# Kernel optimization log

Hardware: AMD Instinct MI355X
Metric: run time of the kernel (lower is better)

## Reference

```python
import jax, jax.numpy as jnp
import numpy as np

R = 4           # max_displacement
P = 2 * R + 1   # search_range = 9
DILATIONS = [[1], [1, 2, 3, 5, 9, 16]]
STRIDES = [4, 1]  # 8 // encoder_output_stride for strides [2, 8]
EPS = 1e-9


def _l2norm(x):
    # torch: x / (x.norm(dim=1, keepdim=True) + 1e-9)
    return x / (jnp.linalg.norm(x, axis=1, keepdims=True) + EPS)


def _corr(x1, x2, dilation, stride):
    """SpatialCorrelationSampler(patch_size=9, stride=stride, padding=0,
    dilation_patch=dilation): out[b,u,v,i,j] = sum_c x1[b,c,i*s,j*s] *
    x2[b,c,i*s+(u-R)*d, j*s+(v-R)*d], zero outside bounds."""
    B, C, H, W = x1.shape
    pad = R * dilation
    x2p = jnp.pad(x2, ((0, 0), (0, 0), (pad, pad), (pad, pad)))
    x1s = x1[:, :, ::stride, ::stride]  # (B,C,Ho,Wo)
    Ho, Wo = x1s.shape[2], x1s.shape[3]
    # all 81 (u,v) patch-offset slice starts in the padded map
    uv = jnp.stack(jnp.meshgrid(jnp.arange(P), jnp.arange(P), indexing='ij'),
                   axis=-1).reshape(-1, 2) * dilation  # (81, 2)

    def step(carry, start):
        x2uv = jax.lax.dynamic_slice(x2p, (0, 0, start[0], start[1]), (B, C, H, W))
        x2uv = x2uv[:, :, ::stride, ::stride]
        return carry, jnp.sum(x1s * x2uv, axis=1)  # (B,Ho,Wo)

    _, cost = jax.lax.scan(step, None, uv)  # (81,B,Ho,Wo)
    cost = cost.reshape(P, P, B, Ho, Wo)
    return jnp.transpose(cost, (2, 0, 1, 3, 4))  # (B,P,P,Ho,Wo)


def setup_inputs() -> dict:
    key = jax.random.key(0)
    k0, k1, k2, k3 = jax.random.split(key, 4)
    return {
        'x1_0': jax.random.normal(k0, (4, 256, 192, 256), dtype=jnp.float32),
        'x1_1': jax.random.normal(k1, (4, 256, 48, 64), dtype=jnp.float32),
        'x2_0': jax.random.normal(k2, (4, 256, 192, 256), dtype=jnp.float32),
        'x2_1': jax.random.normal(k3, (4, 256, 48, 64), dtype=jnp.float32),
    }


def reference(x1_0, x1_1, x2_0, x2_1):
    xs1, xs2 = [x1_0, x1_1], [x2_0, x2_1]
    cost_list = []
    for x1, x2, dils, s in zip(xs1, xs2, DILATIONS, STRIDES):
        x1n = _l2norm(x1)
        x2n = _l2norm(x2)
        per_dil = [_corr(x1n, x2n, d, s) for d in dils]  # each (B,P,P,Ho,Wo)
        # num_groups=1: per-dilation volumes stack into dim 1
        cost_list.append(jnp.stack(per_dil, axis=1))  # (B,nd,P,P,Ho,Wo)
    return jnp.concatenate(cost_list, axis=1)  # (B,7,9,9,48,64)
```

## Files before the change

kernel.cpp:

```cpp
#include <hip/hip_runtime.h>
#include <stdint.h>

#define EPSN 1e-9f

typedef __fp16 f16x8 __attribute__((ext_vector_type(8)));
typedef float f32x4 __attribute__((ext_vector_type(4)));

#define LDS_FENCE()                                        \
  do {                                                     \
    asm volatile("s_waitcnt lgkmcnt(0)" ::: "memory");     \
    __builtin_amdgcn_sched_barrier(0);                     \
  } while (0)


__global__ __launch_bounds__(256) void norms1_kernel(
    const float* __restrict__ x1_1, const float* __restrict__ x2_1,
    float* __restrict__ ws) {
  int p = blockIdx.x * 256 + threadIdx.x;
  const float* src = (p < 12288) ? x1_1 : x2_1;
  int q = (p < 12288) ? p : p - 12288;
  long base = (long)(q / 3072) * 786432 + (q % 3072);
  float ss = 0.f;
#pragma unroll 8
  for (int c = 0; c < 256; ++c) { float v = src[base + (long)c * 3072]; ss += v * v; }
  ws[p] = 1.f / (sqrtf(ss) + EPSN);
}

__global__ __launch_bounds__(256) void gather1_kernel(
    const float* __restrict__ x1, float* __restrict__ x1s) {
  int idx = blockIdx.x * 256 + threadIdx.x;
  int j = idx & 63;
  int i = (idx >> 6) % 48;
  int c = ((idx >> 6) / 48) & 255;
  int b = idx >> 19;
  b = idx / 786432;
  x1s[idx] = x1[(long)b * 12582912 + (long)c * 49152 + (long)(4 * i) * 256 + 4 * j];
}

__global__ __launch_bounds__(256) void corr0_kernel(
    const float* __restrict__ x1b, long BS, long RS, int CS, long CCS,
    const float* __restrict__ x2, float* __restrict__ out) {
  int bx = blockIdx.x;
  int L = (bx & 7) * 96 + (bx >> 3);
  int y = L % 192, b = L / 192;
  int tid = threadIdx.x;
  int w = tid >> 6, lane = tid & 63;
  int i_lo = (y - 1) / 4; if (i_lo < 0) i_lo = 0;
  int i_hi = (y + 4) / 4; if (i_hi > 47) i_hi = 47;
  int NI = i_hi - i_lo + 1;

  __shared__ float red[4][34][64];
  __shared__ float inv2s[264];
  __shared__ float inv1s[3][64];

  float acc[3][9];
#pragma unroll
  for (int r = 0; r < 3; ++r)
#pragma unroll
    for (int v = 0; v < 9; ++v) acc[r][v] = 0.f;
  float sq0 = 0.f, sq1 = 0.f, sq2 = 0.f, sq3 = 0.f;
  float s1[3] = {0.f, 0.f, 0.f};

  const float* x2row = x2 + (long)b * 12582912 + (long)y * 256 + 4 * lane;
  const float* x1p[3];
#pragma unroll
  for (int r = 0; r < 3; ++r) {
    int ir = i_lo + r; if (ir > 47) ir = 47;
    x1p[r] = x1b + (long)b * BS + (long)ir * RS + (long)lane * CS;
  }

#pragma unroll 4
  for (int cc = 0; cc < 64; ++cc) {
    int c = w * 64 + cc;
    long off2 = (long)c * 49152;
    long off1 = (long)c * CCS;
    float4 f = *reinterpret_cast<const float4*>(x2row + off2);
    sq0 += f.x * f.x; sq1 += f.y * f.y; sq2 += f.z * f.z; sq3 += f.w * f.w;
#pragma unroll
    for (int r = 0; r < 3; ++r) {
      float xv = x1p[r][off1];
      float xr = __shfl_down(xv, 1);
      float xl = __shfl_up(xv, 1);
      s1[r] += xv * xv;
      acc[r][0] += xr * f.x; acc[r][1] += xr * f.y;
      acc[r][2] += xr * f.z; acc[r][3] += xr * f.w;
      acc[r][4] += xv * f.x; acc[r][5] += xv * f.y;
      acc[r][6] += xv * f.z; acc[r][7] += xv * f.w;
      acc[r][8] += xl * f.x;
    }
  }

#pragma unroll
  for (int r = 0; r < 3; ++r) {
    red[w][r * 9 + 0][lane] = __shfl_up(acc[r][0], 1);
    red[w][r * 9 + 1][lane] = __shfl_up(acc[r][1], 1);
    red[w][r * 9 + 2][lane] = __shfl_up(acc[r][2], 1);
    red[w][r * 9 + 3][lane] = __shfl_up(acc[r][3], 1);
    red[w][r * 9 + 4][lane] = acc[r][4];
    red[w][r * 9 + 5][lane] = acc[r][5];
    red[w][r * 9 + 6][lane] = acc[r][6];
    red[w][r * 9 + 7][lane] = acc[r][7];
    red[w][r * 9 + 8][lane] = __shfl_down(acc[r][8], 1);
    red[w][31 + r][lane] = s1[r];
  }
  red[w][27][lane] = sq0; red[w][28][lane] = sq1;
  red[w][29][lane] = sq2; red[w][30][lane] = sq3;
  __syncthreads();
  {
    int comp = tid & 3, jj = tid >> 2;
    float ss = red[0][27 + comp][jj] + red[1][27 + comp][jj] +
               red[2][27 + comp][jj] + red[3][27 + comp][jj];
    inv2s[4 + tid] = 1.f / (sqrtf(ss) + EPSN);
    if (tid < 4) { inv2s[tid] = 0.f; inv2s[260 + tid] = 0.f; }
    if (tid < 192) {
      int r = tid >> 6, j = tid & 63;
      float t = red[0][31 + r][j] + red[1][31 + r][j] +
                red[2][31 + r][j] + red[3][31 + r][j];
      inv1s[r][j] = 1.f / (sqrtf(t) + EPSN);
    }
  }
  __syncthreads();
  int lim = NI * 576;
  for (int idx = tid; idx < lim; idx += 256) {
    int r = idx / 576, rem = idx - r * 576;
    int v = rem >> 6, j = rem & 63;
    int i_r = i_lo + r;
    int u_r = y - 4 * i_r + 4;
    float s = red[0][r * 9 + v][j] + red[1][r * 9 + v][j] +
              red[2][r * 9 + v][j] + red[3][r * 9 + v][j];
    out[(long)b * 1741824 + (long)u_r * 27648 + (long)v * 3072 + i_r * 64 + j] =
        s * inv1s[r][j] * inv2s[4 * j + v];
  }
}

__global__ __launch_bounds__(256) void zfill0_kernel(float* __restrict__ out) {
  int idx = blockIdx.x * 256 + threadIdx.x;
  int b = idx / 2880, rem = idx - b * 2880;
  int k = rem / 576, rem2 = rem - k * 576;
  int v = rem2 >> 6, j = rem2 & 63;
  int u = (k < 4) ? k : 8;
  int i = (k < 4) ? 0 : 47;
  out[(long)b * 1741824 + (long)u * 27648 + (long)v * 3072 + i * 64 + j] = 0.f;
}

__global__ __launch_bounds__(256) void xpose1_kernel(
    const float* __restrict__ x1, const float* __restrict__ x2,
    __fp16* __restrict__ o1, __fp16* __restrict__ o2) {
  int bx = blockIdx.x;
  int tz = bx & 1; int rem = bx >> 1;
  int i = rem % 48, b = rem / 48;
  const float* src = tz ? x2 : x1;
  __fp16* dst = (tz ? o2 : o1) + (long)(b * 48 + i) * 16384;
  __shared__ uint32_t lds[64 * 128];
  __shared__ float sred[4][64];
  int t = threadIdx.x;
  int j = t & 63, cg = t >> 6;
  const float* sp = src + (long)b * 786432 + (long)i * 64 + j;
  float vv[64];
  float ss = 0.f;
#pragma unroll
  for (int c8 = 0; c8 < 64; ++c8) {
    float v = sp[(long)(cg * 64 + c8) * 3072];
    vv[c8] = v;
    ss += v * v;
  }
  sred[cg][j] = ss;
  __syncthreads();
  float invv = 1.f / (sqrtf(sred[0][j] + sred[1][j] + sred[2][j] + sred[3][j]) + EPSN);
#pragma unroll
  for (int cb = 0; cb < 8; ++cb) {
    uint32_t pk[4];
#pragma unroll
    for (int e2 = 0; e2 < 4; ++e2) {
      int cl = cb * 8 + e2 * 2;
      __fp16 h0 = (__fp16)(vv[cl] * invv);
      __fp16 h1 = (__fp16)(vv[cl + 1] * invv);
      pk[e2] = (uint32_t)__builtin_bit_cast(uint16_t, h0) |
               ((uint32_t)__builtin_bit_cast(uint16_t, h1) << 16);
    }
    int byteoff = j * 512 + ((cg * 128 + cb * 16) ^ ((j & 7) << 4));
    *reinterpret_cast<uint4*>(reinterpret_cast<char*>(lds) + byteoff) =
        make_uint4(pk[0], pk[1], pk[2], pk[3]);
  }
  __syncthreads();
#pragma unroll
  for (int rep = 0; rep < 8; ++rep) {
    int idx = rep * 256 + t;
    int jj = idx >> 5, cb = idx & 31;
    int byteoff = jj * 512 + ((cb * 16) ^ ((jj & 7) << 4));
    uint4 val = *reinterpret_cast<const uint4*>(
        reinterpret_cast<const char*>(lds) + byteoff);
    *reinterpret_cast<uint4*>(reinterpret_cast<char*>(dst) + jj * 512 + cb * 16) = val;
  }
}

__device__ const int OFFS39[39] = {
    0, 1, -1, 2, -2, 3, -3, 4, -4, 5, -5, 6, -6, 8, -8, 9, -9, 10, -10,
    12, -12, 15, -15, 16, -16, 18, -18, 20, -20, 27, -27, 32, -32, 36, -36,
    48, -48, 64, -64};

__global__ __launch_bounds__(64) void corr1m_kernel(
    const __fp16* __restrict__ w1, const __fp16* __restrict__ w2,
    float* __restrict__ out) {
  const int dils[6] = {1, 2, 3, 5, 9, 16};
  int bx = blockIdx.x;
  int L = (bx & 7) * 936 + (bx >> 3);
  int oi = L % 39, i = (L / 39) % 48, b = L / 1872;
  int o = OFFS39[oi];
  int y = i + o;
  bool valid = (y >= 0 && y < 48);
  int l = threadIdx.x;
  __shared__ float c_lds[64][65];

  if (valid) {
    int lm = l & 15, lk = l >> 4;
    const __fp16* A = w1 + (long)(b * 48 + i) * 16384;
    const __fp16* B = w2 + (long)(b * 48 + y) * 16384;
    f32x4 acc[4][4];
#pragma unroll
    for (int tm = 0; tm < 4; ++tm)
#pragma unroll
      for (int tn = 0; tn < 4; ++tn) acc[tm][tn] = (f32x4)0.f;

    for (int ks = 0; ks < 8; ++ks) {
      f16x8 af[4], bf[4];
      int ko = ks * 32 + lk * 8;
#pragma unroll
      for (int tm = 0; tm < 4; ++tm)
        af[tm] = __builtin_bit_cast(f16x8, *reinterpret_cast<const uint4*>(
                     A + (tm * 16 + lm) * 256 + ko));
#pragma unroll
      for (int tn = 0; tn < 4; ++tn)
        bf[tn] = __builtin_bit_cast(f16x8, *reinterpret_cast<const uint4*>(
                     B + (tn * 16 + lm) * 256 + ko));
#pragma unroll
      for (int tm = 0; tm < 4; ++tm)
#pragma unroll
        for (int tn = 0; tn < 4; ++tn)
          acc[tm][tn] = __builtin_amdgcn_mfma_f32_16x16x32_f16(
              af[tm], bf[tn], acc[tm][tn], 0, 0, 0);
    }
#pragma unroll
    for (int tm = 0; tm < 4; ++tm)
#pragma unroll
      for (int tn = 0; tn < 4; ++tn)
#pragma unroll
        for (int r = 0; r < 4; ++r)
          c_lds[tm * 16 + lk * 4 + r][tn * 16 + lm] = acc[tm][tn][r];
    LDS_FENCE();
  }

#pragma unroll
  for (int dI = 0; dI < 6; ++dI) {
    int d = dils[dI];
    if (o % d) continue;
    int ud = o / d;
    if (ud < -4 || ud > 4) continue;
    long ob = (long)b * 1741824 + (long)(1 + dI) * 248832 +
              (long)(ud + 4) * 27648 + (long)i * 64 + l;
#pragma unroll
    for (int v = 0; v < 9; ++v) {
      float val = 0.f;
      if (valid) {
        int j2 = l + (v - 4) * d;
        val = (j2 >= 0 && j2 < 64) ? c_lds[l][j2] : 0.f;
      }
      out[ob + (long)v * 3072] = val;
    }
  }
}

__global__ __launch_bounds__(64) void corr1_kernel(
    const float* __restrict__ x1, const float* __restrict__ x2,
    const float* __restrict__ ws, float* __restrict__ out) {
  int bx = blockIdx.x;
  int L = (bx & 7) * 1296 + (bx >> 3);
  int u = L % 9, dI = (L / 9) % 6, i = (L / 54) % 48, b = L / 2592;
  const int dils[6] = {1, 2, 3, 5, 9, 16};
  int d = dils[dI];
  int y = i + (u - 4) * d;
  int lane = threadIdx.x;
  long ob = (long)b * 1741824 + (long)(1 + dI) * 248832 + (long)u * 27648 +
            (long)i * 64 + lane;
  if (y < 0 || y >= 48) {
#pragma unroll
    for (int v = 0; v < 9; ++v) out[ob + v * 3072] = 0.f;
    return;
  }
  __shared__ uint4 x2t[192];
  x2t[lane] = make_uint4(0, 0, 0, 0);
  x2t[lane + 64] = make_uint4(0, 0, 0, 0);
  x2t[lane + 128] = make_uint4(0, 0, 0, 0);
  float acc[9];
#pragma unroll
  for (int v = 0; v < 9; ++v) acc[v] = 0.f;
  const float* x2row = x2 + (long)b * 786432 + (long)y * 64 + lane;
  const float* x1row = x1 + (long)b * 786432 + (long)i * 64 + lane;
#pragma unroll 1
  for (int cc8 = 0; cc8 < 32; ++cc8) {
    float x1v[8]; uint32_t xb[8];
#pragma unroll
    for (int cc = 0; cc < 8; ++cc) {
      long c = cc8 * 8 + cc;
      xb[cc] = __float_as_uint(x2row[c * 3072]) + 0x8000u;
      x1v[cc] = x1row[c * 3072];
    }
    uint4 pk;
    pk.x = (xb[0] >> 16) | (xb[1] & 0xffff0000u);
    pk.y = (xb[2] >> 16) | (xb[3] & 0xffff0000u);
    pk.z = (xb[4] >> 16) | (xb[5] & 0xffff0000u);
    pk.w = (xb[6] >> 16) | (xb[7] & 0xffff0000u);
    x2t[64 + lane] = pk;
    LDS_FENCE();
#pragma unroll
    for (int v = 0; v < 9; ++v) {
      uint4 q = x2t[64 + lane + (v - 4) * d];
      float s;
      s  = x1v[0] * __uint_as_float(q.x << 16);
      s += x1v[1] * __uint_as_float(q.x & 0xffff0000u);
      s += x1v[2] * __uint_as_float(q.y << 16);
      s += x1v[3] * __uint_as_float(q.y & 0xffff0000u);
      s += x1v[4] * __uint_as_float(q.z << 16);
      s += x1v[5] * __uint_as_float(q.z & 0xffff0000u);
      s += x1v[6] * __uint_as_float(q.w << 16);
      s += x1v[7] * __uint_as_float(q.w & 0xffff0000u);
      acc[v] += s;
    }
    LDS_FENCE();
  }
  const float* i1 = ws + b * 3072 + i * 64;
  const float* i2 = ws + 12288 + b * 3072 + y * 64;
  float inv1 = i1[lane];
#pragma unroll
  for (int v = 0; v < 9; ++v) {
    int col = lane + (v - 4) * d;
    float i2v = (col >= 0 && col < 64) ? i2[col] : 0.f;
    out[ob + v * 3072] = acc[v] * inv1 * i2v;
  }
}

extern "C" void kernel_launch(void* const* d_in, const int* in_sizes, int n_in,
                              void* d_out, int out_size, void* d_ws, size_t ws_size,
                              hipStream_t stream) {
  const float* x1_0 = (const float*)d_in[0];
  const float* x1_1 = (const float*)d_in[1];
  const float* x2_0 = (const float*)d_in[2];
  const float* x2_1 = (const float*)d_in[3];
  float* out = (float*)d_out;
  float* ws = (float*)d_ws;
  if (ws_size >= 25264128) {
    float* x1s = (float*)((char*)d_ws + 12681216);
    gather1_kernel<<<12288, 256, 0, stream>>>(x1_0, x1s);
    corr0_kernel<<<768, 256, 0, stream>>>(x1s, 786432L, 64L, 1, 3072L,
                                          x2_0, out);
  } else {
    corr0_kernel<<<768, 256, 0, stream>>>(x1_0, 12582912L, 1024L, 4, 49152L,
                                          x2_0, out);
  }
  zfill0_kernel<<<45, 256, 0, stream>>>(out);
  if (ws_size >= 12681216) {
    __fp16* w1h = (__fp16*)((char*)d_ws + 98304);
    __fp16* w2h = w1h + 3145728;
    xpose1_kernel<<<384, 256, 0, stream>>>(x1_1, x2_1, w1h, w2h);
    corr1m_kernel<<<7488, 64, 0, stream>>>(w1h, w2h, out);
  } else {
    norms1_kernel<<<96, 256, 0, stream>>>(x1_1, x2_1, ws);
    corr1_kernel<<<10368, 64, 0, stream>>>(x1_1, x2_1, ws, out);
  }
}
```

Baseline: 118.5 us.

## Split corr0 channel loop across eight waves with two-phase LDS reduction

corr0_kernel now launches 512 threads (8 waves), and each wave handles 32 channels instead of 64. This halves the serial channel loop per thread and adds more waves per block to hide the latency of streaming the large x2_0 tensor. The cross-wave reduction buffer shrinks to 8x14x64 floats and is reused in two passes (14 and 13 accumulator rows), which adds extra barriers and reduction reads. Launch bounds are set to (512,4), which may constrain registers.

```diff
diff --git a/kernel.cpp b/kernel.cpp
--- a/kernel.cpp
+++ b/kernel.cpp
@@ -32,12 +32,11 @@
   int j = idx & 63;
   int i = (idx >> 6) % 48;
   int c = ((idx >> 6) / 48) & 255;
-  int b = idx >> 19;
-  b = idx / 786432;
+  int b = idx / 786432;
   x1s[idx] = x1[(long)b * 12582912 + (long)c * 49152 + (long)(4 * i) * 256 + 4 * j];
 }
 
-__global__ __launch_bounds__(256) void corr0_kernel(
+__global__ __launch_bounds__(512, 4) void corr0_kernel(
     const float* __restrict__ x1b, long BS, long RS, int CS, long CCS,
     const float* __restrict__ x2, float* __restrict__ out) {
   int bx = blockIdx.x;
@@ -49,7 +48,7 @@
   int i_hi = (y + 4) / 4; if (i_hi > 47) i_hi = 47;
   int NI = i_hi - i_lo + 1;
 
-  __shared__ float red[4][34][64];
+  __shared__ float red[8][14][64];
   __shared__ float inv2s[264];
   __shared__ float inv1s[3][64];
 
@@ -70,8 +69,8 @@
   }
 
 #pragma unroll 4
-  for (int cc = 0; cc < 64; ++cc) {
-    int c = w * 64 + cc;
+  for (int cc = 0; cc < 32; ++cc) {
+    int c = w * 32 + cc;
     long off2 = (long)c * 49152;
     long off1 = (long)c * CCS;
     float4 f = *reinterpret_cast<const float4*>(x2row + off2);
@@ -92,44 +91,72 @@
 
 #pragma unroll
   for (int r = 0; r < 3; ++r) {
-    red[w][r * 9 + 0][lane] = __shfl_up(acc[r][0], 1);
-    red[w][r * 9 + 1][lane] = __shfl_up(acc[r][1], 1);
-    red[w][r * 9 + 2][lane] = __shfl_up(acc[r][2], 1);
-    red[w][r * 9 + 3][lane] = __shfl_up(acc[r][3], 1);
-    red[w][r * 9 + 4][lane] = acc[r][4];
-    red[w][r * 9 + 5][lane] = acc[r][5];
-    red[w][r * 9 + 6][lane] = acc[r][6];
-    red[w][r * 9 + 7][lane] = acc[r][7];
-    red[w][r * 9 + 8][lane] = __shfl_down(acc[r][8], 1);
-    red[w][31 + r][lane] = s1[r];
-  }
-  red[w][27][lane] = sq0; red[w][28][lane] = sq1;
-  red[w][29][lane] = sq2; red[w][30][lane] = sq3;
-  __syncthreads();
-  {
+    acc[r][0] = __shfl_up(acc[r][0], 1);
+    acc[r][1] = __shfl_up(acc[r][1], 1);
+    acc[r][2] = __shfl_up(acc[r][2], 1);
+    acc[r][3] = __shfl_up(acc[r][3], 1);
+    acc[r][8] = __shfl_down(acc[r][8], 1);
+  }
+
+  red[w][0][lane] = sq0; red[w][1][lane] = sq1;
+  red[w][2][lane] = sq2; red[w][3][lane] = sq3;
+  red[w][4][lane] = s1[0]; red[w][5][lane] = s1[1]; red[w][6][lane] = s1[2];
+  __syncthreads();
+  if (tid < 256) {
     int comp = tid & 3, jj = tid >> 2;
-    float ss = red[0][27 + comp][jj] + red[1][27 + comp][jj] +
-               red[2][27 + comp][jj] + red[3][27 + comp][jj];
+    float ss = 0.f;
+#pragma unroll
+    for (int ww = 0; ww < 8; ++ww) ss += red[ww][comp][jj];
     inv2s[4 + tid] = 1.f / (sqrtf(ss) + EPSN);
-    if (tid < 4) { inv2s[tid] = 0.f; inv2s[260 + tid] = 0.f; }
-    if (tid < 192) {
-      int r = tid >> 6, j = tid & 63;
-      float t = red[0][31 + r][j] + red[1][31 + r][j] +
-                red[2][31 + r][j] + red[3][31 + r][j];
-      inv1s[r][j] = 1.f / (sqrtf(t) + EPSN);
-    }
-  }
-  __syncthreads();
-  int lim = NI * 576;
-  for (int idx = tid; idx < lim; idx += 256) {
-    int r = idx / 576, rem = idx - r * 576;
-    int v = rem >> 6, j = rem & 63;
-    int i_r = i_lo + r;
-    int u_r = y - 4 * i_r + 4;
-    float s = red[0][r * 9 + v][j] + red[1][r * 9 + v][j] +
-              red[2][r * 9 + v][j] + red[3][r * 9 + v][j];
-    out[(long)b * 1741824 + (long)u_r * 27648 + (long)v * 3072 + i_r * 64 + j] =
-        s * inv1s[r][j] * inv2s[4 * j + v];
+  } else if (tid < 264) {
+    int e = tid - 256;
+    inv2s[(e < 4) ? e : (256 + e)] = 0.f;
+  } else if (tid >= 320) {
+    int r = (tid - 320) >> 6, j = tid & 63;
+    float t = 0.f;
+#pragma unroll
+    for (int ww = 0; ww < 8; ++ww) t += red[ww][4 + r][j];
+    inv1s[r][j] = 1.f / (sqrtf(t) + EPSN);
+  }
+  __syncthreads();
+
+#pragma unroll
+  for (int ar = 0; ar < 14; ++ar) {
+    int r = (ar >= 9) ? 1 : 0, v = ar - r * 9;
+    red[w][ar][lane] = acc[r][v];
+  }
+  __syncthreads();
+  for (int idx = tid; idx < 14 * 64; idx += 512) {
+    int ar = idx >> 6, j = idx & 63;
+    int r = (ar >= 9) ? 1 : 0, v = ar - r * 9;
+    if (r < NI) {
+      float s = 0.f;
+#pragma unroll
+      for (int ww = 0; ww < 8; ++ww) s += red[ww][ar][j];
+      int i_r = i_lo + r, u_r = y - 4 * i_r + 4;
+      out[(long)b * 1741824 + (long)u_r * 27648 + (long)v * 3072 + i_r * 64 + j] =
+          s * inv1s[r][j] * inv2s[4 * j + v];
+    }
+  }
+  __syncthreads();
+
+#pragma unroll
+  for (int ar = 14; ar < 27; ++ar) {
+    int r = (ar >= 18) ? 2 : 1, v = ar - r * 9;
+    red[w][ar - 14][lane] = acc[r][v];
+  }
+  __syncthreads();
+  for (int idx = tid; idx < 13 * 64; idx += 512) {
+    int ar = 14 + (idx >> 6), j = idx & 63;
+    int r = (ar >= 18) ? 2 : 1, v = ar - r * 9;
+    if (r < NI) {
+      float s = 0.f;
+#pragma unroll
+      for (int ww = 0; ww < 8; ++ww) s += red[ww][ar - 14][j];
+      int i_r = i_lo + r, u_r = y - 4 * i_r + 4;
+      out[(long)b * 1741824 + (long)u_r * 27648 + (long)v * 3072 + i_r * 64 + j] =
+          s * inv1s[r][j] * inv2s[4 * j + v];
+    }
   }
 }
 
@@ -351,10 +378,10 @@
   if (ws_size >= 25264128) {
     float* x1s = (float*)((char*)d_ws + 12681216);
     gather1_kernel<<<12288, 256, 0, stream>>>(x1_0, x1s);
-    corr0_kernel<<<768, 256, 0, stream>>>(x1s, 786432L, 64L, 1, 3072L,
+    corr0_kernel<<<768, 512, 0, stream>>>(x1s, 786432L, 64L, 1, 3072L,
                                           x2_0, out);
   } else {
-    corr0_kernel<<<768, 256, 0, stream>>>(x1_0, 12582912L, 1024L, 4, 49152L,
+    corr0_kernel<<<768, 512, 0, stream>>>(x1_0, 12582912L, 1024L, 4, 49152L,
                                           x2_0, out);
   }
   zfill0_kernel<<<45, 256, 0, stream>>>(out);
```

Measured after the change: 129.2 us. 9.0% more time.

## Fuse stride-2 correlation, dilated MFMA correlation and zero-fill into one launch

Applied to the files above, without the earlier changes.

Merges the level-0 correlation kernel, the level-1 multi-dilation MFMA correlation and the border zero-fill into a single kernel that dispatches on block index. The aim is to remove launch gaps and let the small level-1 blocks fill the GPU alongside the 768 level-0 blocks. The MFMA part is also reshaped from one 64-thread wave computing a 64x64 tile to four waves each computing a 16-row strip, which synchronises through a block barrier. In exchange, every block now reserves the larger LDS footprint and the 256-thread launch bound, and three of the four waves sit idle during the output write of the level-1 path.

```diff
diff --git a/kernel.cpp b/kernel.cpp
--- a/kernel.cpp
+++ b/kernel.cpp
@@ -32,115 +32,8 @@
   int j = idx & 63;
   int i = (idx >> 6) % 48;
   int c = ((idx >> 6) / 48) & 255;
-  int b = idx >> 19;
-  b = idx / 786432;
+  int b = idx / 786432;
   x1s[idx] = x1[(long)b * 12582912 + (long)c * 49152 + (long)(4 * i) * 256 + 4 * j];
-}
-
-__global__ __launch_bounds__(256) void corr0_kernel(
-    const float* __restrict__ x1b, long BS, long RS, int CS, long CCS,
-    const float* __restrict__ x2, float* __restrict__ out) {
-  int bx = blockIdx.x;
-  int L = (bx & 7) * 96 + (bx >> 3);
-  int y = L % 192, b = L / 192;
-  int tid = threadIdx.x;
-  int w = tid >> 6, lane = tid & 63;
-  int i_lo = (y - 1) / 4; if (i_lo < 0) i_lo = 0;
-  int i_hi = (y + 4) / 4; if (i_hi > 47) i_hi = 47;
-  int NI = i_hi - i_lo + 1;
-
-  __shared__ float red[4][34][64];
-  __shared__ float inv2s[264];
-  __shared__ float inv1s[3][64];
-
-  float acc[3][9];
-#pragma unroll
-  for (int r = 0; r < 3; ++r)
-#pragma unroll
-    for (int v = 0; v < 9; ++v) acc[r][v] = 0.f;
-  float sq0 = 0.f, sq1 = 0.f, sq2 = 0.f, sq3 = 0.f;
-  float s1[3] = {0.f, 0.f, 0.f};
-
-  const float* x2row = x2 + (long)b * 12582912 + (long)y * 256 + 4 * lane;
-  const float* x1p[3];
-#pragma unroll
-  for (int r = 0; r < 3; ++r) {
-    int ir = i_lo + r; if (ir > 47) ir = 47;
-    x1p[r] = x1b + (long)b * BS + (long)ir * RS + (long)lane * CS;
-  }
-
-#pragma unroll 4
-  for (int cc = 0; cc < 64; ++cc) {
-    int c = w * 64 + cc;
-    long off2 = (long)c * 49152;
-    long off1 = (long)c * CCS;
-    float4 f = *reinterpret_cast<const float4*>(x2row + off2);
-    sq0 += f.x * f.x; sq1 += f.y * f.y; sq2 += f.z * f.z; sq3 += f.w * f.w;
-#pragma unroll
-    for (int r = 0; r < 3; ++r) {
-      float xv = x1p[r][off1];
-      float xr = __shfl_down(xv, 1);
-      float xl = __shfl_up(xv, 1);
-      s1[r] += xv * xv;
-      acc[r][0] += xr * f.x; acc[r][1] += xr * f.y;
-      acc[r][2] += xr * f.z; acc[r][3] += xr * f.w;
-      acc[r][4] += xv * f.x; acc[r][5] += xv * f.y;
-      acc[r][6] += xv * f.z; acc[r][7] += xv * f.w;
-      acc[r][8] += xl * f.x;
-    }
-  }
-
-#pragma unroll
-  for (int r = 0; r < 3; ++r) {
-    red[w][r * 9 + 0][lane] = __shfl_up(acc[r][0], 1);
-    red[w][r * 9 + 1][lane] = __shfl_up(acc[r][1], 1);
-    red[w][r * 9 + 2][lane] = __shfl_up(acc[r][2], 1);
-    red[w][r * 9 + 3][lane] = __shfl_up(acc[r][3], 1);
-    red[w][r * 9 + 4][lane] = acc[r][4];
-    red[w][r * 9 + 5][lane] = acc[r][5];
-    red[w][r * 9 + 6][lane] = acc[r][6];
-    red[w][r * 9 + 7][lane] = acc[r][7];
-    red[w][r * 9 + 8][lane] = __shfl_down(acc[r][8], 1);
-    red[w][31 + r][lane] = s1[r];
-  }
-  red[w][27][lane] = sq0; red[w][28][lane] = sq1;
-  red[w][29][lane] = sq2; red[w][30][lane] = sq3;
-  __syncthreads();
-  {
-    int comp = tid & 3, jj = tid >> 2;
-    float ss = red[0][27 + comp][jj] + red[1][27 + comp][jj] +
-               red[2][27 + comp][jj] + red[3][27 + comp][jj];
-    inv2s[4 + tid] = 1.f / (sqrtf(ss) + EPSN);
-    if (tid < 4) { inv2s[tid] = 0.f; inv2s[260 + tid] = 0.f; }
-    if (tid < 192) {
-      int r = tid >> 6, j = tid & 63;
-      float t = red[0][31 + r][j] + red[1][31 + r][j] +
-                red[2][31 + r][j] + red[3][31 + r][j];
-      inv1s[r][j] = 1.f / (sqrtf(t) + EPSN);
-    }
-  }
-  __syncthreads();
-  int lim = NI * 576;
-  for (int idx = tid; idx < lim; idx += 256) {
-    int r = idx / 576, rem = idx - r * 576;
-    int v = rem >> 6, j = rem & 63;
-    int i_r = i_lo + r;
-    int u_r = y - 4 * i_r + 4;
-    float s = red[0][r * 9 + v][j] + red[1][r * 9 + v][j] +
-              red[2][r * 9 + v][j] + red[3][r * 9 + v][j];
-    out[(long)b * 1741824 + (long)u_r * 27648 + (long)v * 3072 + i_r * 64 + j] =
-        s * inv1s[r][j] * inv2s[4 * j + v];
-  }
-}
-
-__global__ __launch_bounds__(256) void zfill0_kernel(float* __restrict__ out) {
-  int idx = blockIdx.x * 256 + threadIdx.x;
-  int b = idx / 2880, rem = idx - b * 2880;
-  int k = rem / 576, rem2 = rem - k * 576;
-  int v = rem2 >> 6, j = rem2 & 63;
-  int u = (k < 4) ? k : 8;
-  int i = (k < 4) ? 0 : 47;
-  out[(long)b * 1741824 + (long)u * 27648 + (long)v * 3072 + i * 64 + j] = 0.f;
 }
 
 __global__ __launch_bounds__(256) void xpose1_kernel(
@@ -199,6 +92,270 @@
     12, -12, 15, -15, 16, -16, 18, -18, 20, -20, 27, -27, 32, -32, 36, -36,
     48, -48, 64, -64};
 
+__global__ __launch_bounds__(256) void corr_fused_kernel(
+    const float* __restrict__ x1s, const float* __restrict__ x2,
+    const __fp16* __restrict__ w1h, const __fp16* __restrict__ w2h,
+    float* __restrict__ out) {
+  __shared__ float smem[9160];
+  int bxg = blockIdx.x;
+  int tid = threadIdx.x;
+
+  if (bxg < 768) {
+    int L = (bxg & 7) * 96 + (bxg >> 3);
+    int y = L % 192, b = L / 192;
+    int w = tid >> 6, lane = tid & 63;
+    int i_lo = (y - 1) / 4; if (i_lo < 0) i_lo = 0;
+    int i_hi = (y + 4) / 4; if (i_hi > 47) i_hi = 47;
+    int NI = i_hi - i_lo + 1;
+    float (*red)[34][64] = reinterpret_cast<float(*)[34][64]>(smem);
+    float* inv2s = smem + 8704;
+    float (*inv1s)[64] = reinterpret_cast<float(*)[64]>(smem + 8968);
+
+    float acc[3][9];
+#pragma unroll
+    for (int r = 0; r < 3; ++r)
+#pragma unroll
+      for (int v = 0; v < 9; ++v) acc[r][v] = 0.f;
+    float sq0 = 0.f, sq1 = 0.f, sq2 = 0.f, sq3 = 0.f;
+    float s1[3] = {0.f, 0.f, 0.f};
+
+    const float* x2row = x2 + (long)b * 12582912 + (long)y * 256 + 4 * lane;
+    const float* x1p[3];
+#pragma unroll
+    for (int r = 0; r < 3; ++r) {
+      int ir = i_lo + r; if (ir > 47) ir = 47;
+      x1p[r] = x1s + (long)b * 786432 + (long)ir * 64 + lane;
+    }
+
+#pragma unroll 4
+    for (int cc = 0; cc < 64; ++cc) {
+      int c = w * 64 + cc;
+      float4 f = *reinterpret_cast<const float4*>(x2row + (long)c * 49152);
+      long off1 = (long)c * 3072;
+      sq0 += f.x * f.x; sq1 += f.y * f.y; sq2 += f.z * f.z; sq3 += f.w * f.w;
+#pragma unroll
+      for (int r = 0; r < 3; ++r) {
+        float xv = x1p[r][off1];
+        float xr = __shfl_down(xv, 1);
+        float xl = __shfl_up(xv, 1);
+        s1[r] += xv * xv;
+        acc[r][0] += xr * f.x; acc[r][1] += xr * f.y;
+        acc[r][2] += xr * f.z; acc[r][3] += xr * f.w;
+        acc[r][4] += xv * f.x; acc[r][5] += xv * f.y;
+        acc[r][6] += xv * f.z; acc[r][7] += xv * f.w;
+        acc[r][8] += xl * f.x;
+      }
+    }
+
+#pragma unroll
+    for (int r = 0; r < 3; ++r) {
+      red[w][r * 9 + 0][lane] = __shfl_up(acc[r][0], 1);
+      red[w][r * 9 + 1][lane] = __shfl_up(acc[r][1], 1);
+      red[w][r * 9 + 2][lane] = __shfl_up(acc[r][2], 1);
+      red[w][r * 9 + 3][lane] = __shfl_up(acc[r][3], 1);
+      red[w][r * 9 + 4][lane] = acc[r][4];
+      red[w][r * 9 + 5][lane] = acc[r][5];
+      red[w][r * 9 + 6][lane] = acc[r][6];
+      red[w][r * 9 + 7][lane] = acc[r][7];
+      red[w][r * 9 + 8][lane] = __shfl_down(acc[r][8], 1);
+      red[w][31 + r][lane] = s1[r];
+    }
+    red[w][27][lane] = sq0; red[w][28][lane] = sq1;
+    red[w][29][lane] = sq2; red[w][30][lane] = sq3;
+    __syncthreads();
+    {
+      int comp = tid & 3, jj = tid >> 2;
+      float ss = red[0][27 + comp][jj] + red[1][27 + comp][jj] +
+                 red[2][27 + comp][jj] + red[3][27 + comp][jj];
+      inv2s[4 + tid] = 1.f / (sqrtf(ss) + EPSN);
+      if (tid < 4) { inv2s[tid] = 0.f; inv2s[260 + tid] = 0.f; }
+      if (tid < 192) {
+        int r = tid >> 6, j = tid & 63;
+        float t = red[0][31 + r][j] + red[1][31 + r][j] +
+                  red[2][31 + r][j] + red[3][31 + r][j];
+        inv1s[r][j] = 1.f / (sqrtf(t) + EPSN);
+      }
+    }
+    __syncthreads();
+    int lim = NI * 576;
+    for (int idx = tid; idx < lim; idx += 256) {
+      int r = idx / 576, rem = idx - r * 576;
+      int v = rem >> 6, j = rem & 63;
+      int i_r = i_lo + r;
+      int u_r = y - 4 * i_r + 4;
+      float s = red[0][r * 9 + v][j] + red[1][r * 9 + v][j] +
+                red[2][r * 9 + v][j] + red[3][r * 9 + v][j];
+      out[(long)b * 1741824 + (long)u_r * 27648 + (long)v * 3072 + i_r * 64 + j] =
+          s * inv1s[r][j] * inv2s[4 * j + v];
+    }
+  } else if (bxg < 8256) {
+    const int dils[6] = {1, 2, 3, 5, 9, 16};
+    int s = bxg - 768;
+    int L = (s & 7) * 936 + (s >> 3);
+    int oi = L % 39, i = (L / 39) % 48, b = L / 1872;
+    int o = OFFS39[oi];
+    int y = i + o;
+    bool valid = (y >= 0 && y < 48);
+    int l = tid & 63, w = tid >> 6;
+    float (*c_lds)[65] = reinterpret_cast<float(*)[65]>(smem);
+
+    if (valid) {
+      int lm = l & 15, lk = l >> 4;
+      const __fp16* A = w1h + (long)(b * 48 + i) * 16384;
+      const __fp16* B = w2h + (long)(b * 48 + y) * 16384;
+      f32x4 acc[4];
+#pragma unroll
+      for (int tn = 0; tn < 4; ++tn) acc[tn] = (f32x4)0.f;
+      for (int ks = 0; ks < 8; ++ks) {
+        int ko = ks * 32 + lk * 8;
+        f16x8 af = __builtin_bit_cast(f16x8, *reinterpret_cast<const uint4*>(
+                       A + (w * 16 + lm) * 256 + ko));
+#pragma unroll
+        for (int tn = 0; tn < 4; ++tn) {
+          f16x8 bf = __builtin_bit_cast(f16x8, *reinterpret_cast<const uint4*>(
+                         B + (tn * 16 + lm) * 256 + ko));
+          acc[tn] = __builtin_amdgcn_mfma_f32_16x16x32_f16(af, bf, acc[tn], 0, 0, 0);
+        }
+      }
+#pragma unroll
+      for (int tn = 0; tn < 4; ++tn)
+#pragma unroll
+        for (int r = 0; r < 4; ++r)
+          c_lds[w * 16 + lk * 4 + r][tn * 16 + lm] = acc[tn][r];
+    }
+    __syncthreads();
+
+    if (tid < 64) {
+#pragma unroll
+      for (int dI = 0; dI < 6; ++dI) {
+        int d = dils[dI];
+        if (o % d) continue;
+        int ud = o / d;
+        if (ud < -4 || ud > 4) continue;
+        long ob = (long)b * 1741824 + (long)(1 + dI) * 248832 +
+                  (long)(ud + 4) * 27648 + (long)i * 64 + l;
+#pragma unroll
+        for (int v = 0; v < 9; ++v) {
+          float val = 0.f;
+          if (valid) {
+            int j2 = l + (v - 4) * d;
+            val = (j2 >= 0 && j2 < 64) ? c_lds[l][j2] : 0.f;
+          }
+          out[ob + (long)v * 3072] = val;
+        }
+      }
+    }
+  } else {
+    int idx = (bxg - 8256) * 256 + tid;
+    int b = idx / 2880, rem = idx - b * 2880;
+    int k = rem / 576, rem2 = rem - k * 576;
+    int v = rem2 >> 6, j = rem2 & 63;
+    int u = (k < 4) ? k : 8;
+    int i = (k < 4) ? 0 : 47;
+    out[(long)b * 1741824 + (long)u * 27648 + (long)v * 3072 + i * 64 + j] = 0.f;
+  }
+}
+
+__global__ __launch_bounds__(256) void corr0_fb_kernel(
+    const float* __restrict__ x1b, const float* __restrict__ x2,
+    float* __restrict__ out) {
+  int bx = blockIdx.x;
+  int L = (bx & 7) * 96 + (bx >> 3);
+  int y = L % 192, b = L / 192;
+  int tid = threadIdx.x;
+  int w = tid >> 6, lane = tid & 63;
+  int i_lo = (y - 1) / 4; if (i_lo < 0) i_lo = 0;
+  int i_hi = (y + 4) / 4; if (i_hi > 47) i_hi = 47;
+  int NI = i_hi - i_lo + 1;
+  __shared__ float red[4][34][64];
+  __shared__ float inv2s[264];
+  __shared__ float inv1s[3][64];
+  float acc[3][9];
+#pragma unroll
+  for (int r = 0; r < 3; ++r)
+#pragma unroll
+    for (int v = 0; v < 9; ++v) acc[r][v] = 0.f;
+  float sq0 = 0.f, sq1 = 0.f, sq2 = 0.f, sq3 = 0.f;
+  float s1[3] = {0.f, 0.f, 0.f};
+  const float* x2row = x2 + (long)b * 12582912 + (long)y * 256 + 4 * lane;
+  const float* x1p[3];
+#pragma unroll
+  for (int r = 0; r < 3; ++r) {
+    int ir = i_lo + r; if (ir > 47) ir = 47;
+    x1p[r] = x1b + (long)b * 12582912 + (long)ir * 1024 + (long)lane * 4;
+  }
+#pragma unroll 4
+  for (int cc = 0; cc < 64; ++cc) {
+    int c = w * 64 + cc;
+    long off = (long)c * 49152;
+    float4 f = *reinterpret_cast<const float4*>(x2row + off);
+    sq0 += f.x * f.x; sq1 += f.y * f.y; sq2 += f.z * f.z; sq3 += f.w * f.w;
+#pragma unroll
+    for (int r = 0; r < 3; ++r) {
+      float xv = x1p[r][off];
+      float xr = __shfl_down(xv, 1);
+      float xl = __shfl_up(xv, 1);
+      s1[r] += xv * xv;
+      acc[r][0] += xr * f.x; acc[r][1] += xr * f.y;
+      acc[r][2] += xr * f.z; acc[r][3] += xr * f.w;
+      acc[r][4] += xv * f.x; acc[r][5] += xv * f.y;
+      acc[r][6] += xv * f.z; acc[r][7] += xv * f.w;
+      acc[r][8] += xl * f.x;
+    }
+  }
+#pragma unroll
+  for (int r = 0; r < 3; ++r) {
+    red[w][r * 9 + 0][lane] = __shfl_up(acc[r][0], 1);
+    red[w][r * 9 + 1][lane] = __shfl_up(acc[r][1], 1);
+    red[w][r * 9 + 2][lane] = __shfl_up(acc[r][2], 1);
+    red[w][r * 9 + 3][lane] = __shfl_up(acc[r][3], 1);
+    red[w][r * 9 + 4][lane] = acc[r][4];
+    red[w][r * 9 + 5][lane] = acc[r][5];
+    red[w][r * 9 + 6][lane] = acc[r][6];
+    red[w][r * 9 + 7][lane] = acc[r][7];
+    red[w][r * 9 + 8][lane] = __shfl_down(acc[r][8], 1);
+    red[w][31 + r][lane] = s1[r];
+  }
+  red[w][27][lane] = sq0; red[w][28][lane] = sq1;
+  red[w][29][lane] = sq2; red[w][30][lane] = sq3;
+  __syncthreads();
+  {
+    int comp = tid & 3, jj = tid >> 2;
+    float ss = red[0][27 + comp][jj] + red[1][27 + comp][jj] +
+               red[2][27 + comp][jj] + red[3][27 + comp][jj];
+    inv2s[4 + tid] = 1.f / (sqrtf(ss) + EPSN);
+    if (tid < 4) { inv2s[tid] = 0.f; inv2s[260 + tid] = 0.f; }
+    if (tid < 192) {
+      int r = tid >> 6, j = tid & 63;
+      float t = red[0][31 + r][j] + red[1][31 + r][j] +
+                red[2][31 + r][j] + red[3][31 + r][j];
+      inv1s[r][j] = 1.f / (sqrtf(t) + EPSN);
+    }
+  }
+  __syncthreads();
+  int lim = NI * 576;
+  for (int idx = tid; idx < lim; idx += 256) {
+    int r = idx / 576, rem = idx - r * 576;
+    int v = rem >> 6, j = rem & 63;
+    int i_r = i_lo + r;
+    int u_r = y - 4 * i_r + 4;
+    float s = red[0][r * 9 + v][j] + red[1][r * 9 + v][j] +
+              red[2][r * 9 + v][j] + red[3][r * 9 + v][j];
+    out[(long)b * 1741824 + (long)u_r * 27648 + (long)v * 3072 + i_r * 64 + j] =
+        s * inv1s[r][j] * inv2s[4 * j + v];
+  }
+}
+
+__global__ __launch_bounds__(256) void zfill0_kernel(float* __restrict__ out) {
+  int idx = blockIdx.x * 256 + threadIdx.x;
+  int b = idx / 2880, rem = idx - b * 2880;
+  int k = rem / 576, rem2 = rem - k * 576;
+  int v = rem2 >> 6, j = rem2 & 63;
+  int u = (k < 4) ? k : 8;
+  int i = (k < 4) ? 0 : 47;
+  out[(long)b * 1741824 + (long)u * 27648 + (long)v * 3072 + i * 64 + j] = 0.f;
+}
+
 __global__ __launch_bounds__(64) void corr1m_kernel(
     const __fp16* __restrict__ w1, const __fp16* __restrict__ w2,
     float* __restrict__ out) {
@@ -211,7 +368,6 @@
   bool valid = (y >= 0 && y < 48);
   int l = threadIdx.x;
   __shared__ float c_lds[64][65];
-
   if (valid) {
     int lm = l & 15, lk = l >> 4;
     const __fp16* A = w1 + (long)(b * 48 + i) * 16384;
@@ -221,7 +377,6 @@
     for (int tm = 0; tm < 4; ++tm)
 #pragma unroll
       for (int tn = 0; tn < 4; ++tn) acc[tm][tn] = (f32x4)0.f;
-
     for (int ks = 0; ks < 8; ++ks) {
       f16x8 af[4], bf[4];
       int ko = ks * 32 + lk * 8;
@@ -249,7 +404,6 @@
           c_lds[tm * 16 + lk * 4 + r][tn * 16 + lm] = acc[tm][tn][r];
     LDS_FENCE();
   }
-
 #pragma unroll
   for (int dI = 0; dI < 6; ++dI) {
     int d = dils[dI];
@@ -349,21 +503,22 @@
   float* out = (float*)d_out;
   float* ws = (float*)d_ws;
   if (ws_size >= 25264128) {
+    __fp16* w1h = (__fp16*)((char*)d_ws + 98304);
+    __fp16* w2h = w1h + 3145728;
     float* x1s = (float*)((char*)d_ws + 12681216);
     gather1_kernel<<<12288, 256, 0, stream>>>(x1_0, x1s);
-    corr0_kernel<<<768, 256, 0, stream>>>(x1s, 786432L, 64L, 1, 3072L,
-                                          x2_0, out);
-  } else {
-    corr0_kernel<<<768, 256, 0, stream>>>(x1_0, 12582912L, 1024L, 4, 49152L,
-                                          x2_0, out);
-  }
-  zfill0_kernel<<<45, 256, 0, stream>>>(out);
-  if (ws_size >= 12681216) {
+    xpose1_kernel<<<384, 256, 0, stream>>>(x1_1, x2_1, w1h, w2h);
+    corr_fused_kernel<<<8301, 256, 0, stream>>>(x1s, x2_0, w1h, w2h, out);
+  } else if (ws_size >= 12681216) {
     __fp16* w1h = (__fp16*)((char*)d_ws + 98304);
     __fp16* w2h = w1h + 3145728;
+    corr0_fb_kernel<<<768, 256, 0, stream>>>(x1_0, x2_0, out);
+    zfill0_kernel<<<45, 256, 0, stream>>>(out);
     xpose1_kernel<<<384, 256, 0, stream>>>(x1_1, x2_1, w1h, w2h);
     corr1m_kernel<<<7488, 64, 0, stream>>>(w1h, w2h, out);
   } else {
+    corr0_fb_kernel<<<768, 256, 0, stream>>>(x1_0, x2_0, out);
+    zfill0_kernel<<<45, 256, 0, stream>>>(out);
     norms1_kernel<<<96, 256, 0, stream>>>(x1_1, x2_1, ws);
     corr1_kernel<<<10368, 64, 0, stream>>>(x1_1, x2_1, ws, out);
   }
```

New measurement: 160.8 us. 1.36x slower.
